# Kernel tuning notes

Hardware: AMD Instinct MI355X
Metric: run time of the kernel (lower is better)

Reference implementation:

```python
import jax, jax.numpy as jnp
import numpy as np

D_MODEL = 512
D_HEAD = 64
N_HEADS = D_MODEL // D_HEAD  # 8
KSIZE = 7


def setup_inputs() -> dict:
    key = jax.random.key(0)
    k1, k2, k3 = jax.random.split(key, 3)
    x = jax.random.normal(k1, (2, 48, 48, D_MODEL), dtype=jnp.float32)
    # torch Linear(d, 3d, bias=False): y = x @ W.T ; store transposed weight directly
    w_qkv = jax.random.normal(k2, (D_MODEL, 3 * D_MODEL), dtype=jnp.float32) * 0.02
    w_out = jax.random.normal(k3, (D_MODEL, D_MODEL), dtype=jnp.float32) * 0.02
    return {"x": x, "w_qkv": w_qkv, "w_out": w_out}


def _nbhd_idx(L, k):
    # NATTEN semantics: window centered at each pixel, shifted (clamped) to stay
    # fully inside the image near borders. Returns [L, k] absolute indices.
    start = jnp.clip(jnp.arange(L) - k // 2, 0, L - k)
    return start[:, None] + jnp.arange(k)[None, :]


def reference(x, w_qkv, w_out):
    n, h, w, _ = x.shape
    qkv = (x @ w_qkv).reshape(n, h, w, 3, N_HEADS, D_HEAD)
    qkv = jnp.transpose(qkv, (3, 0, 4, 1, 2, 5))  # [3, n, nh, h, w, e]
    q, k, v = qkv[0], qkv[1], qkv[2]
    q = q / jnp.asarray(D_HEAD, q.dtype) ** 0.5

    ih = _nbhd_idx(h, KSIZE)  # [h, k]
    iw = _nbhd_idx(w, KSIZE)  # [w, k]
    IH = ih[:, None, :, None]  # [h,1,k,1]
    IW = iw[None, :, None, :]  # [1,w,1,k]

    # gather per-pixel 2D neighborhoods: [n, nh, h, w, ka, kb, e]
    k_nb = k[:, :, IH, IW, :]
    logits = jnp.einsum('nghwe,nghwabe->nghwab', q, k_nb)
    logits = logits.reshape(n, N_HEADS, h, w, KSIZE * KSIZE)
    attn = jax.nn.softmax(logits, axis=-1).reshape(n, N_HEADS, h, w, KSIZE, KSIZE)

    v_nb = v[:, :, IH, IW, :]
    o = jnp.einsum('nghwab,nghwabe->nghwe', attn, v_nb)  # [n, nh, h, w, e]
    o = jnp.transpose(o, (0, 2, 3, 1, 4)).reshape(n, h, w, N_HEADS * D_HEAD)
    return o @ w_out
```

## Files before the change

kernel.cpp:

```cpp
#include <hip/hip_runtime.h>
#include <hip/hip_bf16.h>

typedef __bf16 bf16x4 __attribute__((ext_vector_type(4)));
typedef __bf16 bf16x8 __attribute__((ext_vector_type(8)));
typedef float f32x4 __attribute__((ext_vector_type(4)));

#define N_PIX 4608
#define D_MODEL 512
#define QKV_N 1536

__device__ __forceinline__ void gload_lds16(const void* g, void* l) {
  __builtin_amdgcn_global_load_lds(
      (const __attribute__((address_space(1))) unsigned int*)g,
      (__attribute__((address_space(3))) unsigned int*)l, 16, 0, 0);
}

__global__ __launch_bounds__(256) void prep_kernel(
    const float* __restrict__ x, const float* __restrict__ wq,
    const float* __restrict__ wo, __bf16* __restrict__ xbf,
    __bf16* __restrict__ wqT, __bf16* __restrict__ woT) {
  int b = blockIdx.x, tid = threadIdx.x;
  if (b < 2304) {
    int i = b * 1024 + tid * 4;
    float4 v = *(const float4*)&x[i];
    bf16x4 o = {(__bf16)v.x, (__bf16)v.y, (__bf16)v.z, (__bf16)v.w};
    *(bf16x4*)&xbf[i] = o;
    return;
  }
  __shared__ float tile[32][33];
  const float* src; __bf16* dst; int R, C, bx, by;
  if (b < 3072) {
    int t = b - 2304; src = wq; dst = wqT; R = 512; C = 1536;
    bx = (t % 48) * 32; by = (t / 48) * 32;
  } else {
    int t = b - 3072; src = wo; dst = woT; R = 512; C = 512;
    bx = (t & 15) * 32; by = (t >> 4) * 32;
  }
  int tx = tid & 31, ty = tid >> 5;
#pragma unroll
  for (int i = 0; i < 32; i += 8)
    tile[ty + i][tx] = src[(by + ty + i) * C + bx + tx];
  __syncthreads();
#pragma unroll
  for (int i = 0; i < 32; i += 8)
    dst[(bx + ty + i) * R + by + tx] = (__bf16)tile[tx][ty + i];
}

template <int BN>
__global__ __launch_bounds__(256) void gemm128_kernel(
    const __bf16* __restrict__ A, const __bf16* __restrict__ Bt,
    void* __restrict__ C, int M, int N, int K, int c_is_f32) {
  constexpr int NT = BN / 32;
  constexpr int BROWS = BN / 4;
  __shared__ __bf16 sA[2][128 * 32];
  __shared__ __bf16 sB[2][BN * 32];
  int tid = threadIdx.x;
  int wv = tid >> 6, lane = tid & 63;
  int quad = lane >> 4, r16 = lane & 15;
  int m0 = blockIdx.y * 128, n0 = blockIdx.x * BN;

  int rA = lane >> 2;
  int kc = (lane & 3) * 8;
  const __bf16* Ag0 = A + (long)(m0 + wv * 32 + rA) * K + kc;
  const __bf16* Ag1 = Ag0 + (long)16 * K;
  const __bf16* Bg0 = Bt + (long)(n0 + wv * BROWS + rA) * K + kc;

  int mw = (wv & 1) * 64, nw = (wv >> 1) * (BN / 2);

  f32x4 acc[4][NT];
#pragma unroll
  for (int mt = 0; mt < 4; ++mt)
#pragma unroll
    for (int nt = 0; nt < NT; ++nt) acc[mt][nt] = f32x4{0.f, 0.f, 0.f, 0.f};

  auto stage = [&](int buf, int k0) {
    gload_lds16(Ag0 + k0, &sA[buf][(wv * 32) * 32]);
    gload_lds16(Ag1 + k0, &sA[buf][(wv * 32 + 16) * 32]);
    gload_lds16(Bg0 + k0, &sB[buf][(wv * BROWS) * 32]);
    if (BROWS == 32)
      gload_lds16(Bg0 + (long)16 * K + k0, &sB[buf][(wv * BROWS + 16) * 32]);
  };

  stage(0, 0);
  int cur = 0;
  for (int k0 = 0; k0 < K; k0 += 32) {
    __syncthreads();
    if (k0 + 32 < K) stage(cur ^ 1, k0 + 32);
    bf16x8 af[4], bfr[NT];
#pragma unroll
    for (int mt = 0; mt < 4; ++mt)
      af[mt] = *(const bf16x8*)&sA[cur][(mw + mt * 16 + r16) * 32 + quad * 8];
#pragma unroll
    for (int nt = 0; nt < NT; ++nt)
      bfr[nt] = *(const bf16x8*)&sB[cur][(nw + nt * 16 + r16) * 32 + quad * 8];
#pragma unroll
    for (int mt = 0; mt < 4; ++mt)
#pragma unroll
      for (int nt = 0; nt < NT; ++nt)
        acc[mt][nt] = __builtin_amdgcn_mfma_f32_16x16x32_bf16(af[mt], bfr[nt], acc[mt][nt], 0, 0, 0);
    cur ^= 1;
  }

  __bf16* Cb = (__bf16*)C;
  float* Cf = (float*)C;
#pragma unroll
  for (int mt = 0; mt < 4; ++mt)
#pragma unroll
    for (int r = 0; r < 4; ++r) {
      int row = m0 + mw + mt * 16 + quad * 4 + r;
#pragma unroll
      for (int nt = 0; nt < NT; ++nt) {
        int col = n0 + nw + nt * 16 + r16;
        float v = acc[mt][nt][r];
        if (c_is_f32) Cf[(long)row * N + col] = v;
        else          Cb[(long)row * N + col] = (__bf16)v;
      }
    }
}

#define KSTR 72
__global__ __launch_bounds__(256) void natten_attn_kernel(
    const __bf16* __restrict__ qkv, __bf16* __restrict__ o) {
  __shared__ __bf16 sK[196 * KSTR];
  __shared__ __bf16 sV[196 * KSTR];
  int tid = threadIdx.x;
  int bid = blockIdx.x;
  int nB = bid / 288;
  int rem = bid - nB * 288;
  int head = rem / 36;
  int tile = rem - head * 36;
  int tr = tile / 6, tc = tile - tr * 6;
  int r0 = tr * 8, c0 = tc * 8;
  int loH = r0 - 3; loH = loH < 0 ? 0 : (loH > 41 ? 41 : loH);
  int loW = c0 - 3; loW = loW < 0 ? 0 : (loW > 41 ? 41 : loW);

  for (int j = tid; j < 196 * 8; j += 256) {
    int rowi = j >> 3, ch = j & 7;
    int rr = rowi / 14, cc = rowi - rr * 14;
    int hh = loH + rr; hh = hh > 47 ? 47 : hh;
    int wp = loW + cc; wp = wp > 47 ? 47 : wp;
    long base = (long)(nB * 2304 + hh * 48 + wp) * QKV_N + head * 64 + ch * 8;
    *(uint4*)&sK[rowi * KSTR + ch * 8] = *(const uint4*)&qkv[base + 512];
    *(uint4*)&sV[rowi * KSTR + ch * 8] = *(const uint4*)&qkv[base + 1024];
  }
  __syncthreads();

  int q = tid >> 2, s = tid & 3;
  int qr = q >> 3, qc = q & 7;
  int h = r0 + qr, w = c0 + qc;
  int pix = nB * 2304 + h * 48 + w;
  int hs = h - 3; hs = hs < 0 ? 0 : (hs > 41 ? 41 : hs); hs -= loH;
  int ws = w - 3; ws = ws < 0 ? 0 : (ws > 41 ? 41 : ws); ws -= loW;
  int base = (hs * 14 + ws) * KSTR + s * 16;

  const bf16x8* qp = (const bf16x8*)&qkv[(long)pix * QKV_N + head * 64 + s * 16];
  bf16x8 q0 = qp[0], q1 = qp[1];
  float qf[16];
#pragma unroll
  for (int t = 0; t < 8; ++t) {
    qf[t] = (float)q0[t] * 0.125f;
    qf[8 + t] = (float)q1[t] * 0.125f;
  }

  float lg[49];
#pragma unroll
  for (int j = 0; j < 49; ++j) {
    int a = j / 7, b = j % 7;
    const bf16x8* kp = (const bf16x8*)&sK[base + (a * 14 + b) * KSTR];
    bf16x8 k0 = kp[0], k1 = kp[1];
    float acc = 0.f;
#pragma unroll
    for (int t = 0; t < 8; ++t) {
      acc = fmaf(qf[t], (float)k0[t], acc);
      acc = fmaf(qf[8 + t], (float)k1[t], acc);
    }
    acc += __shfl_xor(acc, 1);
    acc += __shfl_xor(acc, 2);
    lg[j] = acc;
  }

  float mx = lg[0];
#pragma unroll
  for (int j = 1; j < 49; ++j) mx = fmaxf(mx, lg[j]);
  float sm = 0.f;
#pragma unroll
  for (int j = 0; j < 49; ++j) { lg[j] = __expf(lg[j] - mx); sm += lg[j]; }
  float inv = 1.f / sm;

  float ov[16];
#pragma unroll
  for (int t = 0; t < 16; ++t) ov[t] = 0.f;
#pragma unroll
  for (int j = 0; j < 49; ++j) {
    int a = j / 7, b = j % 7;
    float pj = lg[j] * inv;
    const bf16x8* vp = (const bf16x8*)&sV[base + (a * 14 + b) * KSTR];
    bf16x8 v0 = vp[0], v1 = vp[1];
#pragma unroll
    for (int t = 0; t < 8; ++t) {
      ov[t] = fmaf(pj, (float)v0[t], ov[t]);
      ov[8 + t] = fmaf(pj, (float)v1[t], ov[8 + t]);
    }
  }

  bf16x8 o0, o1;
#pragma unroll
  for (int t = 0; t < 8; ++t) {
    o0[t] = (__bf16)ov[t];
    o1[t] = (__bf16)ov[8 + t];
  }
  bf16x8* op = (bf16x8*)&o[(long)pix * D_MODEL + head * 64 + s * 16];
  op[0] = o0;
  op[1] = o1;
}


extern "C" void kernel_launch(void* const* d_in, const int* in_sizes, int n_in,
                              void* d_out, int out_size, void* d_ws, size_t ws_size,
                              hipStream_t stream) {
  const float* x = (const float*)d_in[0];
  const float* w_qkv = (const float*)d_in[1];
  const float* w_out = (const float*)d_in[2];
  float* out = (float*)d_out;

  __bf16* ws = (__bf16*)d_ws;
  __bf16* xbf   = ws;
  __bf16* wqkvT = xbf + N_PIX * D_MODEL;
  __bf16* woutT = wqkvT + QKV_N * D_MODEL;
  __bf16* qkvb  = woutT + D_MODEL * D_MODEL;
  __bf16* obf   = qkvb + N_PIX * QKV_N;

  prep_kernel<<<3328, 256, 0, stream>>>(x, w_qkv, w_out, xbf, wqkvT, woutT);
  gemm128_kernel<128><<<dim3(QKV_N / 128, N_PIX / 128), 256, 0, stream>>>(
      xbf, wqkvT, qkvb, N_PIX, QKV_N, D_MODEL, 0);
  natten_attn_kernel<<<576, 256, 0, stream>>>(qkvb, obf);
  gemm128_kernel<64><<<dim3(D_MODEL / 64, N_PIX / 128), 256, 0, stream>>>(
      obf, woutT, out, N_PIX, D_MODEL, D_MODEL, 1);
}
```

Measured before the change: 124.3 us.

## Fuse all stages into one persistent cooperative kernel with grid syncs

Replaces four separate launches (prep, QKV GEMM, neighborhood attention, output GEMM) with one cooperative kernel of 256 persistent blocks. Stages are separated by grid.sync() and share one LDS buffer. The 1/sqrt(d) query scale is folded into the transposed Q weights during prep, so the attention kernel no longer multiplies Q. This removes launch gaps between stages, but runs only 256 blocks, one per CU, which lowers occupancy and leaves wave imbalance (e.g. 432 GEMM tiles spread over 256 blocks).

```diff
diff --git a/kernel.cpp b/kernel.cpp
--- a/kernel.cpp
+++ b/kernel.cpp
@@ -1,5 +1,8 @@
 #include <hip/hip_runtime.h>
 #include <hip/hip_bf16.h>
+#include <hip/hip_cooperative_groups.h>
+
+namespace cg = cooperative_groups;
 
 typedef __bf16 bf16x4 __attribute__((ext_vector_type(4)));
 typedef __bf16 bf16x8 __attribute__((ext_vector_type(8)));
@@ -8,6 +11,8 @@
 #define N_PIX 4608
 #define D_MODEL 512
 #define QKV_N 1536
+#define KSTR 72
+#define GRID_BLKS 256
 
 __device__ __forceinline__ void gload_lds16(const void* g, void* l) {
   __builtin_amdgcn_global_load_lds(
@@ -15,70 +20,33 @@
       (__attribute__((address_space(3))) unsigned int*)l, 16, 0, 0);
 }
 
-__global__ __launch_bounds__(256) void prep_kernel(
-    const float* __restrict__ x, const float* __restrict__ wq,
-    const float* __restrict__ wo, __bf16* __restrict__ xbf,
-    __bf16* __restrict__ wqT, __bf16* __restrict__ woT) {
-  int b = blockIdx.x, tid = threadIdx.x;
-  if (b < 2304) {
-    int i = b * 1024 + tid * 4;
-    float4 v = *(const float4*)&x[i];
-    bf16x4 o = {(__bf16)v.x, (__bf16)v.y, (__bf16)v.z, (__bf16)v.w};
-    *(bf16x4*)&xbf[i] = o;
-    return;
-  }
-  __shared__ float tile[32][33];
-  const float* src; __bf16* dst; int R, C, bx, by;
-  if (b < 3072) {
-    int t = b - 2304; src = wq; dst = wqT; R = 512; C = 1536;
-    bx = (t % 48) * 32; by = (t / 48) * 32;
-  } else {
-    int t = b - 3072; src = wo; dst = woT; R = 512; C = 512;
-    bx = (t & 15) * 32; by = (t >> 4) * 32;
-  }
-  int tx = tid & 31, ty = tid >> 5;
-#pragma unroll
-  for (int i = 0; i < 32; i += 8)
-    tile[ty + i][tx] = src[(by + ty + i) * C + bx + tx];
-  __syncthreads();
-#pragma unroll
-  for (int i = 0; i < 32; i += 8)
-    dst[(bx + ty + i) * R + by + tx] = (__bf16)tile[tx][ty + i];
-}
-
-template <int BN>
-__global__ __launch_bounds__(256) void gemm128_kernel(
+template <int BM, int BN>
+__device__ __forceinline__ void gemm_tile(
     const __bf16* __restrict__ A, const __bf16* __restrict__ Bt,
-    void* __restrict__ C, int M, int N, int K, int c_is_f32) {
-  constexpr int NT = BN / 32;
-  constexpr int BROWS = BN / 4;
-  __shared__ __bf16 sA[2][128 * 32];
-  __shared__ __bf16 sB[2][BN * 32];
-  int tid = threadIdx.x;
+    void* __restrict__ C, int N, int K, int c_is_f32,
+    int m0, int n0, __bf16* sA, __bf16* sB, int tid) {
+  constexpr int MT = BM / 32, NT = BN / 32, AR = BM / 4, BR = BN / 4;
   int wv = tid >> 6, lane = tid & 63;
   int quad = lane >> 4, r16 = lane & 15;
-  int m0 = blockIdx.y * 128, n0 = blockIdx.x * BN;
-
   int rA = lane >> 2;
   int kc = (lane & 3) * 8;
-  const __bf16* Ag0 = A + (long)(m0 + wv * 32 + rA) * K + kc;
-  const __bf16* Ag1 = Ag0 + (long)16 * K;
-  const __bf16* Bg0 = Bt + (long)(n0 + wv * BROWS + rA) * K + kc;
-
-  int mw = (wv & 1) * 64, nw = (wv >> 1) * (BN / 2);
-
-  f32x4 acc[4][NT];
-#pragma unroll
-  for (int mt = 0; mt < 4; ++mt)
+  const __bf16* Ag0 = A + (long)(m0 + wv * AR + rA) * K + kc;
+  const __bf16* Bg0 = Bt + (long)(n0 + wv * BR + rA) * K + kc;
+  int mw = (wv & 1) * (BM / 2), nw = (wv >> 1) * (BN / 2);
+
+  f32x4 acc[MT][NT];
+#pragma unroll
+  for (int mt = 0; mt < MT; ++mt)
 #pragma unroll
     for (int nt = 0; nt < NT; ++nt) acc[mt][nt] = f32x4{0.f, 0.f, 0.f, 0.f};
 
   auto stage = [&](int buf, int k0) {
-    gload_lds16(Ag0 + k0, &sA[buf][(wv * 32) * 32]);
-    gload_lds16(Ag1 + k0, &sA[buf][(wv * 32 + 16) * 32]);
-    gload_lds16(Bg0 + k0, &sB[buf][(wv * BROWS) * 32]);
-    if (BROWS == 32)
-      gload_lds16(Bg0 + (long)16 * K + k0, &sB[buf][(wv * BROWS + 16) * 32]);
+    gload_lds16(Ag0 + k0, &sA[buf * BM * 32 + (wv * AR) * 32]);
+    if (AR == 32)
+      gload_lds16(Ag0 + (long)16 * K + k0, &sA[buf * BM * 32 + (wv * AR + 16) * 32]);
+    gload_lds16(Bg0 + k0, &sB[buf * BN * 32 + (wv * BR) * 32]);
+    if (BR == 32)
+      gload_lds16(Bg0 + (long)16 * K + k0, &sB[buf * BN * 32 + (wv * BR + 16) * 32]);
   };
 
   stage(0, 0);
@@ -86,15 +54,15 @@
   for (int k0 = 0; k0 < K; k0 += 32) {
     __syncthreads();
     if (k0 + 32 < K) stage(cur ^ 1, k0 + 32);
-    bf16x8 af[4], bfr[NT];
-#pragma unroll
-    for (int mt = 0; mt < 4; ++mt)
-      af[mt] = *(const bf16x8*)&sA[cur][(mw + mt * 16 + r16) * 32 + quad * 8];
+    bf16x8 af[MT], bfr[NT];
+#pragma unroll
+    for (int mt = 0; mt < MT; ++mt)
+      af[mt] = *(const bf16x8*)&sA[cur * BM * 32 + (mw + mt * 16 + r16) * 32 + quad * 8];
 #pragma unroll
     for (int nt = 0; nt < NT; ++nt)
-      bfr[nt] = *(const bf16x8*)&sB[cur][(nw + nt * 16 + r16) * 32 + quad * 8];
-#pragma unroll
-    for (int mt = 0; mt < 4; ++mt)
+      bfr[nt] = *(const bf16x8*)&sB[cur * BN * 32 + (nw + nt * 16 + r16) * 32 + quad * 8];
+#pragma unroll
+    for (int mt = 0; mt < MT; ++mt)
 #pragma unroll
       for (int nt = 0; nt < NT; ++nt)
         acc[mt][nt] = __builtin_amdgcn_mfma_f32_16x16x32_bf16(af[mt], bfr[nt], acc[mt][nt], 0, 0, 0);
@@ -104,7 +72,7 @@
   __bf16* Cb = (__bf16*)C;
   float* Cf = (float*)C;
 #pragma unroll
-  for (int mt = 0; mt < 4; ++mt)
+  for (int mt = 0; mt < MT; ++mt)
 #pragma unroll
     for (int r = 0; r < 4; ++r) {
       int row = m0 + mw + mt * 16 + quad * 4 + r;
@@ -118,15 +86,11 @@
     }
 }
 
-#define KSTR 72
-__global__ __launch_bounds__(256) void natten_attn_kernel(
-    const __bf16* __restrict__ qkv, __bf16* __restrict__ o) {
-  __shared__ __bf16 sK[196 * KSTR];
-  __shared__ __bf16 sV[196 * KSTR];
-  int tid = threadIdx.x;
-  int bid = blockIdx.x;
-  int nB = bid / 288;
-  int rem = bid - nB * 288;
+__device__ __forceinline__ void attn_tile(
+    const __bf16* __restrict__ qkvb, __bf16* __restrict__ obf,
+    int it, int tid, __bf16* sK, __bf16* sV) {
+  int nB = it / 288;
+  int rem = it - nB * 288;
   int head = rem / 36;
   int tile = rem - head * 36;
   int tr = tile / 6, tc = tile - tr * 6;
@@ -140,8 +104,8 @@
     int hh = loH + rr; hh = hh > 47 ? 47 : hh;
     int wp = loW + cc; wp = wp > 47 ? 47 : wp;
     long base = (long)(nB * 2304 + hh * 48 + wp) * QKV_N + head * 64 + ch * 8;
-    *(uint4*)&sK[rowi * KSTR + ch * 8] = *(const uint4*)&qkv[base + 512];
-    *(uint4*)&sV[rowi * KSTR + ch * 8] = *(const uint4*)&qkv[base + 1024];
+    *(uint4*)&sK[rowi * KSTR + ch * 8] = *(const uint4*)&qkvb[base + 512];
+    *(uint4*)&sV[rowi * KSTR + ch * 8] = *(const uint4*)&qkvb[base + 1024];
   }
   __syncthreads();
 
@@ -153,13 +117,13 @@
   int ws = w - 3; ws = ws < 0 ? 0 : (ws > 41 ? 41 : ws); ws -= loW;
   int base = (hs * 14 + ws) * KSTR + s * 16;
 
-  const bf16x8* qp = (const bf16x8*)&qkv[(long)pix * QKV_N + head * 64 + s * 16];
+  const bf16x8* qp = (const bf16x8*)&qkvb[(long)pix * QKV_N + head * 64 + s * 16];
   bf16x8 q0 = qp[0], q1 = qp[1];
   float qf[16];
 #pragma unroll
   for (int t = 0; t < 8; ++t) {
-    qf[t] = (float)q0[t] * 0.125f;
-    qf[8 + t] = (float)q1[t] * 0.125f;
+    qf[t] = (float)q0[t];
+    qf[8 + t] = (float)q1[t];
   }
 
   float lg[49];
@@ -209,9 +173,110 @@
     o0[t] = (__bf16)ov[t];
     o1[t] = (__bf16)ov[8 + t];
   }
-  bf16x8* op = (bf16x8*)&o[(long)pix * D_MODEL + head * 64 + s * 16];
+  bf16x8* op = (bf16x8*)&obf[(long)pix * D_MODEL + head * 64 + s * 16];
   op[0] = o0;
   op[1] = o1;
+}
+
+__device__ __forceinline__ void prep_item(
+    const float* __restrict__ x, const float* __restrict__ wq,
+    const float* __restrict__ wo, __bf16* __restrict__ xbf,
+    __bf16* __restrict__ wqT, __bf16* __restrict__ woT,
+    int b, int tid, float(*ptile)[33]) {
+  if (b < 2304) {
+    int i = b * 1024 + tid * 4;
+    float4 v = *(const float4*)&x[i];
+    bf16x4 o = {(__bf16)v.x, (__bf16)v.y, (__bf16)v.z, (__bf16)v.w};
+    *(bf16x4*)&xbf[i] = o;
+    return;
+  }
+  const float* src; __bf16* dst; int C, bx, by;
+  bool is_wq;
+  if (b < 3072) {
+    int t = b - 2304; src = wq; dst = wqT; C = 1536;
+    bx = (t % 48) * 32; by = (t / 48) * 32; is_wq = true;
+  } else {
+    int t = b - 3072; src = wo; dst = woT; C = 512;
+    bx = (t & 15) * 32; by = (t >> 4) * 32; is_wq = false;
+  }
+  int tx = tid & 31, ty = tid >> 5;
+  __syncthreads();
+#pragma unroll
+  for (int i = 0; i < 32; i += 8)
+    ptile[ty + i][tx] = src[(by + ty + i) * C + bx + tx];
+  __syncthreads();
+#pragma unroll
+  for (int i = 0; i < 32; i += 8) {
+    int outrow = bx + ty + i;
+    float v = ptile[tx][ty + i];
+    if (is_wq && outrow < 512) v *= 0.125f;
+    dst[outrow * 512 + by + tx] = (__bf16)v;
+  }
+}
+
+__global__ __launch_bounds__(256) void natten_fused_kernel(
+    const float* __restrict__ x, const float* __restrict__ wq,
+    const float* __restrict__ wo, float* __restrict__ out,
+    __bf16* __restrict__ xbf, __bf16* __restrict__ wqT,
+    __bf16* __restrict__ woT, __bf16* __restrict__ qkvb,
+    __bf16* __restrict__ obf) {
+  cg::grid_group grid = cg::this_grid();
+  __shared__ __align__(16) char shmem[2 * 196 * KSTR * sizeof(__bf16)];
+  __bf16* sK = (__bf16*)shmem;
+  __bf16* sV = (__bf16*)(shmem + 196 * KSTR * sizeof(__bf16));
+  __bf16* sA = (__bf16*)shmem;
+  __bf16* sB = (__bf16*)(shmem + 16384);
+  float(*ptile)[33] = (float(*)[33])shmem;
+
+  int bid = blockIdx.x, tid = threadIdx.x;
+
+  for (int b = bid; b < 3328; b += GRID_BLKS)
+    prep_item(x, wq, wo, xbf, wqT, woT, b, tid, ptile);
+  grid.sync();
+
+  for (int t = bid; t < 432; t += GRID_BLKS) {
+    __syncthreads();
+    gemm_tile<128, 128>(xbf, wqT, qkvb, QKV_N, D_MODEL, 0,
+                        (t / 12) * 128, (t % 12) * 128, sA, sB, tid);
+  }
+  grid.sync();
+
+  for (int it = bid; it < 576; it += GRID_BLKS) {
+    __syncthreads();
+    attn_tile(qkvb, obf, it, tid, sK, sV);
+  }
+  grid.sync();
+
+  for (int t = bid; t < 288; t += GRID_BLKS) {
+    __syncthreads();
+    gemm_tile<128, 64>(obf, woT, out, D_MODEL, D_MODEL, 1,
+                       (t / 8) * 128, (t % 8) * 64, sA, sB, tid);
+  }
+}
+
+__global__ __launch_bounds__(256) void prep_kernel(
+    const float* __restrict__ x, const float* __restrict__ wq,
+    const float* __restrict__ wo, __bf16* __restrict__ xbf,
+    __bf16* __restrict__ wqT, __bf16* __restrict__ woT) {
+  __shared__ float ptile[32][33];
+  prep_item(x, wq, wo, xbf, wqT, woT, blockIdx.x, threadIdx.x, ptile);
+}
+
+template <int BM, int BN>
+__global__ __launch_bounds__(256) void gemm_kernel(
+    const __bf16* __restrict__ A, const __bf16* __restrict__ Bt,
+    void* __restrict__ C, int N, int K, int c_is_f32) {
+  __shared__ __bf16 sA[2 * BM * 32];
+  __shared__ __bf16 sB[2 * BN * 32];
+  gemm_tile<BM, BN>(A, Bt, C, N, K, c_is_f32,
+                    blockIdx.y * BM, blockIdx.x * BN, sA, sB, threadIdx.x);
+}
+
+__global__ __launch_bounds__(256) void natten_attn_kernel(
+    const __bf16* __restrict__ qkvb, __bf16* __restrict__ obf) {
+  __shared__ __bf16 sK[196 * KSTR];
+  __shared__ __bf16 sV[196 * KSTR];
+  attn_tile(qkvb, obf, blockIdx.x, threadIdx.x, sK, sV);
 }
 
 
@@ -219,21 +284,27 @@
                               void* d_out, int out_size, void* d_ws, size_t ws_size,
                               hipStream_t stream) {
   const float* x = (const float*)d_in[0];
-  const float* w_qkv = (const float*)d_in[1];
-  const float* w_out = (const float*)d_in[2];
+  const float* wq = (const float*)d_in[1];
+  const float* wo = (const float*)d_in[2];
   float* out = (float*)d_out;
 
   __bf16* ws = (__bf16*)d_ws;
-  __bf16* xbf   = ws;
-  __bf16* wqkvT = xbf + N_PIX * D_MODEL;
-  __bf16* woutT = wqkvT + QKV_N * D_MODEL;
-  __bf16* qkvb  = woutT + D_MODEL * D_MODEL;
-  __bf16* obf   = qkvb + N_PIX * QKV_N;
-
-  prep_kernel<<<3328, 256, 0, stream>>>(x, w_qkv, w_out, xbf, wqkvT, woutT);
-  gemm128_kernel<128><<<dim3(QKV_N / 128, N_PIX / 128), 256, 0, stream>>>(
-      xbf, wqkvT, qkvb, N_PIX, QKV_N, D_MODEL, 0);
-  natten_attn_kernel<<<576, 256, 0, stream>>>(qkvb, obf);
-  gemm128_kernel<64><<<dim3(D_MODEL / 64, N_PIX / 128), 256, 0, stream>>>(
-      obf, woutT, out, N_PIX, D_MODEL, D_MODEL, 1);
-}
+  __bf16* xbf  = ws;
+  __bf16* wqT  = xbf + N_PIX * D_MODEL;
+  __bf16* woT  = wqT + QKV_N * D_MODEL;
+  __bf16* qkvb = woT + D_MODEL * D_MODEL;
+  __bf16* obf  = qkvb + N_PIX * QKV_N;
+
+  void* args[] = {(void*)&x, (void*)&wq, (void*)&wo, (void*)&out,
+                  (void*)&xbf, (void*)&wqT, (void*)&woT, (void*)&qkvb, (void*)&obf};
+  hipError_t err = hipLaunchCooperativeKernel(
+      (void*)natten_fused_kernel, dim3(GRID_BLKS), dim3(256), args, 0, stream);
+  if (err != hipSuccess) {
+    prep_kernel<<<3328, 256, 0, stream>>>(x, wq, wo, xbf, wqT, woT);
+    gemm_kernel<128, 128><<<dim3(QKV_N / 128, N_PIX / 128), 256, 0, stream>>>(
+        xbf, wqT, qkvb, QKV_N, D_MODEL, 0);
+    natten_attn_kernel<<<576, 256, 0, stream>>>(qkvb, obf);
+    gemm_kernel<128, 64><<<dim3(D_MODEL / 64, N_PIX / 128), 256, 0, stream>>>(
+        obf, woT, out, D_MODEL, D_MODEL, 1);
+  }
+}
```

After: 234.9 us. 1.89x slower.
